# Kernel optimization log

Measured on AMD Instinct MI355X. Metric: run time of the kernel, lower is better.

The kernel has to match this reference:

```python
import jax, jax.numpy as jnp
from jax import lax
import numpy as np

LOWEST_HZ = 1.0
HIGHEST_HZ = 40.0
FS = 256
ORDER = 5


def _butter_sos(order, cutoff, btype, fs):
    """Butterworth digital filter as second-order sections (scipy-equivalent math)."""
    Wn = cutoff / (0.5 * fs)
    fs2 = 2.0
    warped = 2.0 * fs2 * np.tan(np.pi * Wn / fs2)  # pre-warped analog cutoff
    m = np.arange(1, order + 1)
    p = np.exp(1j * np.pi * (2 * m + order - 1) / (2.0 * order))  # analog prototype poles
    if btype == 'lp':
        z = np.zeros(0, dtype=complex)
        p = p * warped
        k = warped ** order
    else:  # 'hp' : lp2hp transform
        k = 1.0 / np.real(np.prod(-p))
        p = warped / p
        z = np.zeros(order, dtype=complex)
    # bilinear transform (internal fs = 2)
    f2 = 2.0 * fs2
    pd = (f2 + p) / (f2 - p)
    zd = (f2 + z) / (f2 - z)
    kd = k * np.real(np.prod(f2 - z) / np.prod(f2 - p))
    zd = np.concatenate([zd, -np.ones(order - len(zd))])  # pad zeros at z=-1
    z0 = float(np.real(zd[0]))  # all digital zeros identical (z=-1 for lp, z=+1 for hp)
    real_p = [float(pp.real) for pp in pd if abs(pp.imag) < 1e-10]
    cplx_p = [pp for pp in pd if pp.imag > 1e-10]
    sos = []
    for pp in cplx_p:  # conjugate pair -> one biquad
        sos.append([1.0, -2.0 * z0, z0 * z0, 1.0, -2.0 * pp.real, float(np.real(pp * np.conj(pp)))])
    for pr in real_p:  # leftover real pole -> first-order section
        sos.append([1.0, -z0, 0.0, 1.0, -pr, 0.0])
    sos = np.array(sos, dtype=np.float64)
    sos[0, :3] *= kd  # fold overall gain into first section
    return sos


def _sosfilt(sos, x):
    """Cascaded biquad IIR (direct form II transposed), zero initial state. x: [..., T]."""
    S = sos.shape[0]
    b0, b1, b2 = sos[:, 0], sos[:, 1], sos[:, 2]
    a1, a2 = sos[:, 4], sos[:, 5]
    xT = jnp.moveaxis(x, -1, 0)  # [T, ...]
    state0 = jnp.zeros((S, 2) + xT.shape[1:], x.dtype)

    def step(state, xt):
        cur = xt
        new = []
        for i in range(S):  # fixed small cascade of 6 sections
            w1, w2 = state[i, 0], state[i, 1]
            y = b0[i] * cur + w1
            nw1 = b1[i] * cur - a1[i] * y + w2
            nw2 = b2[i] * cur - a2[i] * y
            new.append(jnp.stack([nw1, nw2]))
            cur = y
        return jnp.stack(new), cur

    _, yT = lax.scan(step, state0, xT)
    return jnp.moveaxis(yT, 0, -1)


def setup_inputs() -> dict:
    key = jax.random.key(0)
    x = jax.random.normal(key, (32, 64, 16384), dtype=jnp.float32)
    sos_hp = _butter_sos(ORDER, LOWEST_HZ, 'hp', FS)
    sos_lp = _butter_sos(ORDER, HIGHEST_HZ, 'lp', FS)
    sos = jnp.asarray(np.concatenate([sos_hp, sos_lp], axis=0), dtype=jnp.float32)  # [6,6]
    return {"x": x, "sos": sos}


def reference(x, sos):
    # highpass sections then lowpass sections = one 6-section cascade
    return _sosfilt(sos, x)
```

## Files before the change

kernel.cpp:

```cpp
#include <hip/hip_runtime.h>

#define T_LEN 16384
#define L_BLK 64
#define K_BLK (T_LEN / L_BLK)
#define NSEC 6
#define NSTATE (2 * NSEC)
#define NPOW 8
#define NS_TOT 2048
#define NMAT (NSTATE * NSTATE)

__device__ float g_Mp[NPOW * NMAT];

__global__ void k_matpow(const float* __restrict__ sos) {
    __shared__ double A[NMAT];
    int tid = threadIdx.x;

    if (tid < NSTATE) {
        double b0[NSEC], b1[NSEC], b2[NSEC], a1[NSEC], a2[NSEC];
#pragma unroll
        for (int i = 0; i < NSEC; ++i) {
            b0[i] = (double)sos[i * 6 + 0];
            b1[i] = (double)sos[i * 6 + 1];
            b2[i] = (double)sos[i * 6 + 2];
            a1[i] = (double)sos[i * 6 + 4];
            a2[i] = (double)sos[i * 6 + 5];
        }
        double w1[NSEC], w2[NSEC];
#pragma unroll
        for (int i = 0; i < NSEC; ++i) {
            w1[i] = (tid == 2 * i) ? 1.0 : 0.0;
            w2[i] = (tid == 2 * i + 1) ? 1.0 : 0.0;
        }
        double cur = 0.0;
#pragma unroll
        for (int i = 0; i < NSEC; ++i) {
            double y = fma(b0[i], cur, w1[i]);
            double nw1 = fma(b1[i], cur, fma(-a1[i], y, w2[i]));
            double nw2 = fma(b2[i], cur, -(a2[i] * y));
            w1[i] = nw1; w2[i] = nw2; cur = y;
        }
#pragma unroll
        for (int i = 0; i < NSEC; ++i) {
            A[(2 * i) * NSTATE + tid]     = w1[i];
            A[(2 * i + 1) * NSTATE + tid] = w2[i];
        }
    }
    __syncthreads();

    int r = tid / NSTATE, c = tid % NSTATE;
    for (int it = 1; it <= 13; ++it) {
        double v = 0.0;
        if (tid < NMAT) {
#pragma unroll
            for (int k = 0; k < NSTATE; ++k)
                v = fma(A[r * NSTATE + k], A[k * NSTATE + c], v);
        }
        __syncthreads();
        if (tid < NMAT) {
            A[r * NSTATE + c] = v;
            if (it >= 6) g_Mp[(it - 6) * NMAT + tid] = (float)v;
        }
        __syncthreads();
    }
}

__global__ void __launch_bounds__(K_BLK, 4) k_main(const float* __restrict__ x,
                                                   const float* __restrict__ sos,
                                                   float* __restrict__ y) {
    __shared__ float Mp[NPOW][NMAT];
    __shared__ float cbuf[K_BLK][NSTATE + 1];
    int sig = blockIdx.x;
    int k = threadIdx.x;

    for (int i = k; i < NPOW * NMAT; i += K_BLK)
        Mp[i / NMAT][i % NMAT] = g_Mp[i];

    float b0[NSEC], b1[NSEC], b2[NSEC], a1[NSEC], a2[NSEC];
#pragma unroll
    for (int i = 0; i < NSEC; ++i) {
        b0[i] = sos[i * 6 + 0];
        b1[i] = sos[i * 6 + 1];
        b2[i] = sos[i * 6 + 2];
        a1[i] = sos[i * 6 + 4];
        a2[i] = sos[i * 6 + 5];
    }

    const float* xp = x + (size_t)sig * T_LEN + (size_t)k * L_BLK;

    float4 stash[L_BLK / 4];
    float w1[NSEC], w2[NSEC];
#pragma unroll
    for (int i = 0; i < NSEC; ++i) { w1[i] = 0.f; w2[i] = 0.f; }
#pragma unroll
    for (int t4 = 0; t4 < L_BLK / 4; ++t4) {
        float4 v = *reinterpret_cast<const float4*>(xp + 4 * t4);
        stash[t4] = v;
        float in4[4] = {v.x, v.y, v.z, v.w};
#pragma unroll
        for (int q = 0; q < 4; ++q) {
            float cur = in4[q];
#pragma unroll
            for (int i = 0; i < NSEC; ++i) {
                float yv = fmaf(b0[i], cur, w1[i]);
                w1[i] = fmaf(b1[i], cur, fmaf(-a1[i], yv, w2[i]));
                w2[i] = fmaf(b2[i], cur, -(a2[i] * yv));
                cur = yv;
            }
        }
    }
    float c[NSTATE];
#pragma unroll
    for (int i = 0; i < NSEC; ++i) { c[2 * i] = w1[i]; c[2 * i + 1] = w2[i]; }

    __syncthreads();

#pragma unroll
    for (int rnd = 0; rnd < NPOW; ++rnd) {
        int d = 1 << rnd;
#pragma unroll
        for (int j = 0; j < NSTATE; ++j) cbuf[k][j] = c[j];
        __syncthreads();
        if (k >= d) {
            float prev[NSTATE];
#pragma unroll
            for (int j = 0; j < NSTATE; ++j) prev[j] = cbuf[k - d][j];
            float nc[NSTATE];
#pragma unroll
            for (int r = 0; r < NSTATE; ++r) {
                float acc = c[r];
#pragma unroll
                for (int kk = 0; kk < NSTATE; ++kk)
                    acc = fmaf(Mp[rnd][r * NSTATE + kk], prev[kk], acc);
                nc[r] = acc;
            }
#pragma unroll
            for (int j = 0; j < NSTATE; ++j) c[j] = nc[j];
        }
        __syncthreads();
    }

#pragma unroll
    for (int j = 0; j < NSTATE; ++j) cbuf[k][j] = c[j];
    __syncthreads();
#pragma unroll
    for (int i = 0; i < NSEC; ++i) {
        w1[i] = (k == 0) ? 0.f : cbuf[k - 1][2 * i];
        w2[i] = (k == 0) ? 0.f : cbuf[k - 1][2 * i + 1];
    }

    float* yp = y + (size_t)sig * T_LEN + (size_t)k * L_BLK;
#pragma unroll
    for (int t4 = 0; t4 < L_BLK / 4; ++t4) {
        float4 v = stash[t4];
        float in4[4] = {v.x, v.y, v.z, v.w};
        float out4[4];
#pragma unroll
        for (int q = 0; q < 4; ++q) {
            float cur = in4[q];
#pragma unroll
            for (int i = 0; i < NSEC; ++i) {
                float yv = fmaf(b0[i], cur, w1[i]);
                w1[i] = fmaf(b1[i], cur, fmaf(-a1[i], yv, w2[i]));
                w2[i] = fmaf(b2[i], cur, -(a2[i] * yv));
                cur = yv;
            }
            out4[q] = cur;
        }
        *reinterpret_cast<float4*>(yp + 4 * t4) = make_float4(out4[0], out4[1], out4[2], out4[3]);
    }
}

extern "C" void kernel_launch(void* const* d_in, const int* in_sizes, int n_in,
                              void* d_out, int out_size, void* d_ws, size_t ws_size,
                              hipStream_t stream) {
    const float* x   = (const float*)d_in[0];
    const float* sos = (const float*)d_in[1];
    if (n_in >= 2 && in_sizes[0] <= 256 && in_sizes[1] > 256) {
        x = (const float*)d_in[1];
        sos = (const float*)d_in[0];
    }
    float* out = (float*)d_out;

    int NS = out_size / T_LEN;
    if (NS > NS_TOT) NS = NS_TOT;
    if (NS < 1) NS = 1;

    k_matpow<<<1, 256, 0, stream>>>(sos);
    k_main<<<NS, K_BLK, 0, stream>>>(x, sos, out);
}
```

Measured before the change: 122.1 us.

## Fuse matrix-power setup into main kernel and stage IO through swizzled LDS

```diff
diff --git a/kernel.cpp b/kernel.cpp
--- a/kernel.cpp
+++ b/kernel.cpp
@@ -1,172 +1,180 @@
 #include <hip/hip_runtime.h>
 
 #define T_LEN 16384
-#define L_BLK 64
-#define K_BLK (T_LEN / L_BLK)
 #define NSEC 6
-#define NSTATE (2 * NSEC)
+#define NSTATE 12
+#define NMAT (NSTATE * NSTATE)
 #define NPOW 8
+#define NTHR 512
 #define NS_TOT 2048
-#define NMAT (NSTATE * NSTATE)
 
-__device__ float g_Mp[NPOW * NMAT];
-
-__global__ void k_matpow(const float* __restrict__ sos) {
-    __shared__ double A[NMAT];
-    int tid = threadIdx.x;
-
-    if (tid < NSTATE) {
-        double b0[NSEC], b1[NSEC], b2[NSEC], a1[NSEC], a2[NSEC];
-#pragma unroll
-        for (int i = 0; i < NSEC; ++i) {
-            b0[i] = (double)sos[i * 6 + 0];
-            b1[i] = (double)sos[i * 6 + 1];
-            b2[i] = (double)sos[i * 6 + 2];
-            a1[i] = (double)sos[i * 6 + 4];
-            a2[i] = (double)sos[i * 6 + 5];
-        }
-        double w1[NSEC], w2[NSEC];
-#pragma unroll
-        for (int i = 0; i < NSEC; ++i) {
-            w1[i] = (tid == 2 * i) ? 1.0 : 0.0;
-            w2[i] = (tid == 2 * i + 1) ? 1.0 : 0.0;
-        }
-        double cur = 0.0;
-#pragma unroll
-        for (int i = 0; i < NSEC; ++i) {
-            double y = fma(b0[i], cur, w1[i]);
-            double nw1 = fma(b1[i], cur, fma(-a1[i], y, w2[i]));
-            double nw2 = fma(b2[i], cur, -(a2[i] * y));
-            w1[i] = nw1; w2[i] = nw2; cur = y;
-        }
-#pragma unroll
-        for (int i = 0; i < NSEC; ++i) {
-            A[(2 * i) * NSTATE + tid]     = w1[i];
-            A[(2 * i + 1) * NSTATE + tid] = w2[i];
-        }
-    }
-    __syncthreads();
-
-    int r = tid / NSTATE, c = tid % NSTATE;
-    for (int it = 1; it <= 13; ++it) {
-        double v = 0.0;
-        if (tid < NMAT) {
-#pragma unroll
-            for (int k = 0; k < NSTATE; ++k)
-                v = fma(A[r * NSTATE + k], A[k * NSTATE + c], v);
-        }
-        __syncthreads();
-        if (tid < NMAT) {
-            A[r * NSTATE + c] = v;
-            if (it >= 6) g_Mp[(it - 6) * NMAT + tid] = (float)v;
-        }
-        __syncthreads();
-    }
+__device__ __forceinline__ float rfl(float v) {
+    return __int_as_float(__builtin_amdgcn_readfirstlane(__float_as_int(v)));
+}
+__device__ __forceinline__ int swz(int f) {
+    return (f & ~15) | ((f ^ (f >> 4)) & 15);
 }
 
-__global__ void __launch_bounds__(K_BLK, 4) k_main(const float* __restrict__ x,
-                                                   const float* __restrict__ sos,
-                                                   float* __restrict__ y) {
-    __shared__ float Mp[NPOW][NMAT];
-    __shared__ float cbuf[K_BLK][NSTATE + 1];
-    int sig = blockIdx.x;
-    int k = threadIdx.x;
+__global__ void __launch_bounds__(NTHR, 4)
+k_main(const float* __restrict__ x, const float* __restrict__ sos,
+       float* __restrict__ y) {
+    __shared__ float  Mp[NPOW][NMAT];
+    __shared__ double Ad[NMAT];
+    __shared__ float4 sm4[1664];
+    float* cb = (float*)sm4;
 
-    for (int i = k; i < NPOW * NMAT; i += K_BLK)
-        Mp[i / NMAT][i % NMAT] = g_Mp[i];
+    const int k = threadIdx.x;
+    const int t = k & 255;
+    const int h = k >> 8;
+    const int sig0 = blockIdx.x * 2;
 
     float b0[NSEC], b1[NSEC], b2[NSEC], a1[NSEC], a2[NSEC];
 #pragma unroll
     for (int i = 0; i < NSEC; ++i) {
-        b0[i] = sos[i * 6 + 0];
-        b1[i] = sos[i * 6 + 1];
-        b2[i] = sos[i * 6 + 2];
-        a1[i] = sos[i * 6 + 4];
-        a2[i] = sos[i * 6 + 5];
+        b0[i] = rfl(sos[i * 6 + 0]);
+        b1[i] = rfl(sos[i * 6 + 1]);
+        b2[i] = rfl(sos[i * 6 + 2]);
+        a1[i] = rfl(sos[i * 6 + 4]);
+        a2[i] = rfl(sos[i * 6 + 5]);
     }
 
-    const float* xp = x + (size_t)sig * T_LEN + (size_t)k * L_BLK;
-
-    float4 stash[L_BLK / 4];
-    float w1[NSEC], w2[NSEC];
+    if (k < NSTATE) {
+        float w1[NSEC], w2[NSEC];
 #pragma unroll
-    for (int i = 0; i < NSEC; ++i) { w1[i] = 0.f; w2[i] = 0.f; }
+        for (int i = 0; i < NSEC; ++i) {
+            w1[i] = (k == 2 * i) ? 1.f : 0.f;
+            w2[i] = (k == 2 * i + 1) ? 1.f : 0.f;
+        }
+        float cur = 0.f;
 #pragma unroll
-    for (int t4 = 0; t4 < L_BLK / 4; ++t4) {
-        float4 v = *reinterpret_cast<const float4*>(xp + 4 * t4);
-        stash[t4] = v;
-        float in4[4] = {v.x, v.y, v.z, v.w};
+        for (int i = 0; i < NSEC; ++i) {
+            float yv = fmaf(b0[i], cur, w1[i]);
+            float n1 = fmaf(b1[i], cur, fmaf(-a1[i], yv, w2[i]));
+            float n2 = fmaf(b2[i], cur, -(a2[i] * yv));
+            w1[i] = n1; w2[i] = n2; cur = yv;
+        }
 #pragma unroll
-        for (int q = 0; q < 4; ++q) {
-            float cur = in4[q];
-#pragma unroll
-            for (int i = 0; i < NSEC; ++i) {
-                float yv = fmaf(b0[i], cur, w1[i]);
-                w1[i] = fmaf(b1[i], cur, fmaf(-a1[i], yv, w2[i]));
-                w2[i] = fmaf(b2[i], cur, -(a2[i] * yv));
-                cur = yv;
-            }
+        for (int i = 0; i < NSEC; ++i) {
+            Ad[(2 * i) * NSTATE + k]     = (double)w1[i];
+            Ad[(2 * i + 1) * NSTATE + k] = (double)w2[i];
         }
     }
-    float c[NSTATE];
+    __syncthreads();
+    {
+        const int rr = k / NSTATE, cc = k % NSTATE;
+        for (int it = 1; it <= 13; ++it) {
+            double v = 0.0;
+            if (k < NMAT) {
 #pragma unroll
-    for (int i = 0; i < NSEC; ++i) { c[2 * i] = w1[i]; c[2 * i + 1] = w2[i]; }
+                for (int kk = 0; kk < NSTATE; ++kk)
+                    v = fma(Ad[rr * NSTATE + kk], Ad[kk * NSTATE + cc], v);
+            }
+            __syncthreads();
+            if (k < NMAT) {
+                Ad[rr * NSTATE + cc] = v;
+                if (it >= 6) Mp[it - 6][k] = (float)v;
+            }
+            __syncthreads();
+        }
+    }
+
+    float4 stash[16];
+#pragma unroll 1
+    for (int r = 0; r < 8; ++r) {
+        const int hr = r >> 2, c = r & 3;
+        const float4* src = (const float4*)(x + (size_t)(sig0 + hr) * T_LEN + (c << 12));
+        float4 v0 = src[k];
+        float4 v1 = src[k + 512];
+        __syncthreads();
+        sm4[swz(k)]       = v0;
+        sm4[swz(k + 512)] = v1;
+        __syncthreads();
+        if (h == hr && (t >> 6) == c) {
+            const int tp = t & 63;
+#pragma unroll
+            for (int m = 0; m < 16; ++m)
+                stash[m] = sm4[tp * 16 + (m ^ (tp & 15))];
+        }
+    }
+
+    float w1_[NSEC], w2_[NSEC];
+#pragma unroll
+    for (int i = 0; i < NSEC; ++i) { w1_[i] = 0.f; w2_[i] = 0.f; }
+
+    auto fstep = [&](float cur) -> float {
+#pragma unroll
+        for (int i = 0; i < NSEC; ++i) {
+            float yv = fmaf(b0[i], cur, w1_[i]);
+            w1_[i] = fmaf(b1[i], cur, fmaf(-a1[i], yv, w2_[i]));
+            w2_[i] = fmaf(b2[i], cur, -(a2[i] * yv));
+            cur = yv;
+        }
+        return cur;
+    };
+
+#pragma unroll
+    for (int m = 0; m < 16; ++m) {
+        float4 v = stash[m];
+        fstep(v.x); fstep(v.y); fstep(v.z); fstep(v.w);
+    }
+    float c0[NSTATE];
+#pragma unroll
+    for (int i = 0; i < NSEC; ++i) { c0[2 * i] = w1_[i]; c0[2 * i + 1] = w2_[i]; }
 
     __syncthreads();
-
+#pragma unroll 1
+    for (int rnd = 0; rnd < NPOW; ++rnd) {
+        const int d = 1 << rnd;
 #pragma unroll
-    for (int rnd = 0; rnd < NPOW; ++rnd) {
-        int d = 1 << rnd;
+        for (int j = 0; j < NSTATE; ++j) cb[k * 13 + j] = c0[j];
+        __syncthreads();
+        if (t >= d) {
+            float pr[NSTATE], nc[NSTATE];
 #pragma unroll
-        for (int j = 0; j < NSTATE; ++j) cbuf[k][j] = c[j];
-        __syncthreads();
-        if (k >= d) {
-            float prev[NSTATE];
+            for (int j = 0; j < NSTATE; ++j) pr[j] = cb[(k - d) * 13 + j];
 #pragma unroll
-            for (int j = 0; j < NSTATE; ++j) prev[j] = cbuf[k - d][j];
-            float nc[NSTATE];
-#pragma unroll
-            for (int r = 0; r < NSTATE; ++r) {
-                float acc = c[r];
+            for (int q = 0; q < NSTATE; ++q) {
+                float acc = c0[q];
 #pragma unroll
                 for (int kk = 0; kk < NSTATE; ++kk)
-                    acc = fmaf(Mp[rnd][r * NSTATE + kk], prev[kk], acc);
-                nc[r] = acc;
+                    acc = fmaf(Mp[rnd][q * NSTATE + kk], pr[kk], acc);
+                nc[q] = acc;
             }
 #pragma unroll
-            for (int j = 0; j < NSTATE; ++j) c[j] = nc[j];
+            for (int j = 0; j < NSTATE; ++j) c0[j] = nc[j];
         }
         __syncthreads();
     }
-
 #pragma unroll
-    for (int j = 0; j < NSTATE; ++j) cbuf[k][j] = c[j];
+    for (int j = 0; j < NSTATE; ++j) cb[k * 13 + j] = c0[j];
     __syncthreads();
 #pragma unroll
     for (int i = 0; i < NSEC; ++i) {
-        w1[i] = (k == 0) ? 0.f : cbuf[k - 1][2 * i];
-        w2[i] = (k == 0) ? 0.f : cbuf[k - 1][2 * i + 1];
+        w1_[i] = (t == 0) ? 0.f : cb[(k - 1) * 13 + 2 * i];
+        w2_[i] = (t == 0) ? 0.f : cb[(k - 1) * 13 + 2 * i + 1];
     }
 
-    float* yp = y + (size_t)sig * T_LEN + (size_t)k * L_BLK;
 #pragma unroll
-    for (int t4 = 0; t4 < L_BLK / 4; ++t4) {
-        float4 v = stash[t4];
-        float in4[4] = {v.x, v.y, v.z, v.w};
-        float out4[4];
+    for (int m = 0; m < 16; ++m) {
+        float4 v = stash[m];
+        v.x = fstep(v.x); v.y = fstep(v.y); v.z = fstep(v.z); v.w = fstep(v.w);
+        stash[m] = v;
+    }
+
+#pragma unroll 1
+    for (int r = 0; r < 8; ++r) {
+        const int hr = r >> 2, c = r & 3;
+        __syncthreads();
+        if (h == hr && (t >> 6) == c) {
+            const int tp = t & 63;
 #pragma unroll
-        for (int q = 0; q < 4; ++q) {
-            float cur = in4[q];
-#pragma unroll
-            for (int i = 0; i < NSEC; ++i) {
-                float yv = fmaf(b0[i], cur, w1[i]);
-                w1[i] = fmaf(b1[i], cur, fmaf(-a1[i], yv, w2[i]));
-                w2[i] = fmaf(b2[i], cur, -(a2[i] * yv));
-                cur = yv;
-            }
-            out4[q] = cur;
+            for (int m = 0; m < 16; ++m)
+                sm4[tp * 16 + (m ^ (tp & 15))] = stash[m];
         }
-        *reinterpret_cast<float4*>(yp + 4 * t4) = make_float4(out4[0], out4[1], out4[2], out4[3]);
+        __syncthreads();
+        float4* dst = (float4*)(y + (size_t)(sig0 + hr) * T_LEN + (c << 12));
+        dst[k]       = sm4[swz(k)];
+        dst[k + 512] = sm4[swz(k + 512)];
     }
 }
 
@@ -183,8 +191,7 @@
 
     int NS = out_size / T_LEN;
     if (NS > NS_TOT) NS = NS_TOT;
-    if (NS < 1) NS = 1;
+    if (NS < 2) NS = 2;
 
-    k_matpow<<<1, 256, 0, stream>>>(sos);
-    k_main<<<NS, K_BLK, 0, stream>>>(x, sos, out);
+    k_main<<<NS / 2, NTHR, 0, stream>>>(x, sos, out);
 }
```

Measured after the change: 118.4 us. -3.0%, faster.
